# Kernel optimization log

Hardware: AMD Instinct MI355X
Metric: run time of the kernel (lower is better)

Reference implementation:

```python
import jax, jax.numpy as jnp
import numpy as np

DIM = 256
NUM_HEADS = 8
BALL_SIZE = 16
DIMENSIONALITY = 3
TOPK = 2  # hardcoded in the torch forward
NM = 8192  # n_balls(512) * ball_size(16)


def setup_inputs() -> dict:
    key = jax.random.key(0)
    ks = jax.random.split(key, 6)
    s = 0.02
    return {
        "x": jax.random.normal(ks[0], (NM, DIM), jnp.float32),
        "pos": jax.random.normal(ks[1], (NM, DIMENSIONALITY), jnp.float32),
        "W_qkv": jax.random.normal(ks[2], (3 * DIM, DIM), jnp.float32) * s,
        "b_qkv": jnp.zeros((3 * DIM,), jnp.float32),
        "W_pe": jax.random.normal(ks[3], (DIM, DIMENSIONALITY), jnp.float32) * s,
        "b_pe": jnp.zeros((DIM,), jnp.float32),
        "W_proj": jax.random.normal(ks[4], (DIM, DIM), jnp.float32) * s,
        "b_proj": jnp.zeros((DIM,), jnp.float32),
    }


def reference(x, pos, W_qkv, b_qkv, W_pe, b_pe, W_proj, b_proj):
    M, H, K = BALL_SIZE, NUM_HEADS, TOPK
    nm, dim = x.shape
    n = nm // M
    E = dim // H

    # relative positions wrt ball center (torch version is under no_grad)
    p = jax.lax.stop_gradient(pos).reshape(n, M, -1)
    rel = (p - p.mean(axis=1, keepdims=True)).reshape(nm, -1)
    x = x + rel @ W_pe.T + b_pe

    # qkv: '(n m) (H E K) -> K n H m E'  (K is innermost in the split)
    qkv = (x @ W_qkv.T + b_qkv).reshape(n, M, H, E, 3)
    qkv = jnp.transpose(qkv, (4, 0, 2, 1, 3))  # [3, n, H, m, E]
    q, k, v = qkv[0], qkv[1], qkv[2]

    qf = jnp.transpose(q, (1, 0, 2, 3)).reshape(H, nm, E)  # H (n m) E
    kh = jnp.transpose(k, (1, 0, 2, 3))  # H n m E
    vh = jnp.transpose(v, (1, 0, 2, 3))  # H n m E

    # per-ball key means, query-ball similarity, top-k ball selection
    kmean = kh.mean(axis=2)                          # H n E
    sim = jnp.einsum('hqe,hne->hqn', qf, kmean)      # H nm n
    _, idx = jax.lax.top_k(sim, K)                   # H nm K

    # gather selected balls' keys/values per (head, query-token)
    dk = jax.vmap(lambda kk, ii: kk[ii])(kh, idx).reshape(H, nm, K * M, E)
    dv = jax.vmap(lambda vv, ii: vv[ii])(vh, idx).reshape(H, nm, K * M, E)

    logits = jnp.einsum('hqe,hqke->hqk', qf, dk) / jnp.sqrt(jnp.float32(E))
    attn = jax.nn.softmax(logits, axis=-1)           # H nm (K*m)
    out = jnp.einsum('hqk,hqke->hqe', attn, dv)      # H nm E
    out = jnp.transpose(out, (1, 0, 2)).reshape(nm, dim)  # nm (H E)
    return out @ W_proj.T + b_proj
```

## Files before the change

### kernel.cpp

```cpp
#include <hip/hip_runtime.h>

#define DIM 256
#define NH 8
#define HE 32
#define BALL 16
#define NBALLS 512
#define NM 8192

typedef _Float16 f16x8 __attribute__((ext_vector_type(8)));
typedef float f32x4 __attribute__((ext_vector_type(4)));

__device__ __forceinline__ void f2h_split(float val, _Float16& hi,
                                          _Float16& lo) {
  hi = (_Float16)val;
  lo = (_Float16)(val - (float)hi);
}

__device__ __forceinline__ void gld_lds16(_Float16* lds, const _Float16* g) {
  __builtin_amdgcn_global_load_lds(
      (const __attribute__((address_space(1))) unsigned int*)g,
      (__attribute__((address_space(3))) unsigned int*)lds, 16, 0, 0);
}

__global__ __launch_bounds__(256) void k_prep(
    const float* __restrict__ x, const float* __restrict__ pos,
    const float* __restrict__ Wpe, const float* __restrict__ bpe,
    _Float16* __restrict__ xcat, const float* __restrict__ Wq,
    const float* __restrict__ Wp, _Float16* __restrict__ Bq,
    _Float16* __restrict__ Bp) {
  if (blockIdx.x >= NBALLS) {
    int n = blockIdx.x - NBALLS;
    int k = threadIdx.x;
    if (n < 768) {
      _Float16 hi, lo;
      f2h_split(Wq[n * 256 + k], hi, lo);
      Bq[n * 768 + k] = hi;
      Bq[n * 768 + 256 + k] = hi;
      Bq[n * 768 + 512 + k] = lo;
    } else {
      int r = n - 768;
      _Float16 hi, lo;
      f2h_split(Wp[r * 256 + k], hi, lo);
      Bp[r * 768 + k] = hi;
      Bp[r * 768 + 256 + k] = hi;
      Bp[r * 768 + 512 + k] = lo;
    }
    return;
  }
  __shared__ float ps[BALL * 3];
  __shared__ float mean_s[3];
  int ball = blockIdx.x;
  int tid = threadIdx.x;
  if (tid < BALL * 3) ps[tid] = pos[ball * BALL * 3 + tid];
  __syncthreads();
  if (tid < 3) {
    float s = 0.f;
    for (int m = 0; m < BALL; ++m) s += ps[m * 3 + tid];
    mean_s[tid] = s * (1.f / BALL);
  }
  __syncthreads();
  int d = tid;
  float w0 = Wpe[d * 3 + 0], w1 = Wpe[d * 3 + 1], w2 = Wpe[d * 3 + 2];
  float bp = bpe[d];
  float m0 = mean_s[0], m1 = mean_s[1], m2 = mean_s[2];
  for (int m = 0; m < BALL; ++m) {
    int t = ball * BALL + m;
    float r0 = ps[m * 3 + 0] - m0;
    float r1 = ps[m * 3 + 1] - m1;
    float r2 = ps[m * 3 + 2] - m2;
    float val = x[t * DIM + d] + r0 * w0 + r1 * w1 + r2 * w2 + bp;
    _Float16 hi, lo;
    f2h_split(val, hi, lo);
    xcat[t * 512 + d] = hi;
    xcat[t * 512 + 256 + d] = lo;
  }
}

#define TBK 64

template <typename AF, typename BF, typename Epi>
__device__ __forceinline__ void gemm_core(AF a_addr, BF b_addr,
                                          const float* __restrict__ bias,
                                          int m0, int n0, Epi epi) {
  __shared__ _Float16 As[128 * 64];
  __shared__ _Float16 Bs[64 * 64];
  int tid = threadIdx.x;
  int w = tid >> 6, lane = tid & 63;
  int wm = (w >> 1) * 64, wn = (w & 1) * 32;
  int l15 = lane & 15, quad = lane >> 4;
  int sw = l15 & 7;
  f32x4 acc[4][2] = {};
  for (int k0 = 0; k0 < 768; k0 += TBK) {
    int ak0 = (k0 < 512) ? k0 : (k0 - 512);
    if (k0) __syncthreads();
#pragma unroll
    for (int t = 0; t < 4; ++t) {
      int f = tid + 256 * t;
      int row = f >> 3, sg = (f & 7) ^ (row & 7);
      gld_lds16(&As[f * 8], a_addr(m0 + row, ak0 + sg * 8));
    }
#pragma unroll
    for (int t = 0; t < 2; ++t) {
      int f = tid + 256 * t;
      int row = f >> 3, sg = (f & 7) ^ (row & 7);
      gld_lds16(&Bs[f * 8], b_addr(n0 + row, k0 + sg * 8));
    }
    __syncthreads();
#pragma unroll
    for (int kk = 0; kk < TBK; kk += 32) {
      int ls = (kk >> 3) + quad;
      int psg = (ls ^ sw) * 8;
      f16x8 bfr0 = *(const f16x8*)&Bs[(wn + l15) * 64 + psg];
      f16x8 bfr1 = *(const f16x8*)&Bs[(wn + 16 + l15) * 64 + psg];
#pragma unroll
      for (int mt = 0; mt < 4; ++mt) {
        f16x8 afr = *(const f16x8*)&As[(wm + mt * 16 + l15) * 64 + psg];
        acc[mt][0] = __builtin_amdgcn_mfma_f32_16x16x32_f16(afr, bfr0,
                                                            acc[mt][0], 0, 0,
                                                            0);
        acc[mt][1] = __builtin_amdgcn_mfma_f32_16x16x32_f16(afr, bfr1,
                                                            acc[mt][1], 0, 0,
                                                            0);
      }
    }
  }
#pragma unroll
  for (int mt = 0; mt < 4; ++mt) {
#pragma unroll
    for (int nt = 0; nt < 2; ++nt) {
      int col = n0 + wn + nt * 16 + l15;
      float bv = bias[col];
#pragma unroll
      for (int r = 0; r < 4; ++r) {
        int row = m0 + wm + mt * 16 + quad * 4 + r;
        epi(row, col, acc[mt][nt][r] + bv);
      }
    }
  }
}

__global__ __launch_bounds__(256) void k_qkv_gemm(
    const _Float16* __restrict__ A, const _Float16* __restrict__ B,
    const float* __restrict__ bias, _Float16* __restrict__ qcat,
    float* __restrict__ kbuf, _Float16* __restrict__ kv16) {
  int m0 = blockIdx.x * 128, n0 = blockIdx.y * 64;
  gemm_core(
      [=](int r, int k) { return &A[r * 512 + k]; },
      [=](int r, int k) { return &B[r * 768 + k]; }, bias, m0, n0,
      [=](int row, int col, float val) {
        int c = col % 3;
        int rr = col / 3;
        int e = rr & 31;
        int h = rr >> 5;
        if (c == 0) {
          _Float16 hi, lo;
          f2h_split(val, hi, lo);
          qcat[(h * NM + row) * 64 + e] = hi;
          qcat[(h * NM + row) * 64 + 32 + e] = lo;
        } else if (c == 1) {
          kbuf[(h * NM + row) * HE + e] = val;
          kv16[(h * NM + row) * 64 + e] = (_Float16)val;
        } else {
          kv16[(h * NM + row) * 64 + 32 + e] = (_Float16)val;
        }
      });
}

__global__ __launch_bounds__(256) void k_proj(
    const _Float16* __restrict__ acat, const _Float16* __restrict__ B,
    const float* __restrict__ bias, float* __restrict__ out) {
  int m0 = blockIdx.x * 128, n0 = blockIdx.y * 64;
  gemm_core(
      [=](int r, int k) {
        int half = k >> 8, hh = (k >> 5) & 7, e0 = k & 31;
        return &acat[((half * NH + hh) * NM + r) * 32 + e0];
      },
      [=](int r, int k) { return &B[r * 768 + k]; }, bias, m0, n0,
      [=](int row, int col, float val) { out[row * DIM + col] = val; });
}

__global__ __launch_bounds__(256) void k_kmean(
    const float* __restrict__ kbuf, _Float16* __restrict__ kmc) {
  int tid = threadIdx.x;
  int gb = blockIdx.x * 8 + (tid >> 5);
  int e = tid & 31;
  int h = gb >> 9, ball = gb & 511;
  float s = 0.f;
#pragma unroll
  for (int m = 0; m < BALL; ++m)
    s += kbuf[(h * NM + ball * BALL + m) * HE + e];
  float mean = s * (1.f / BALL);
  _Float16 hi, lo;
  f2h_split(mean, hi, lo);
  kmc[gb * 64 + e] = hi;
  kmc[gb * 64 + 32 + e] = lo;
}

__global__ __launch_bounds__(512) void k_sim_topk(
    const _Float16* __restrict__ qcat, const _Float16* __restrict__ kmc,
    int2* __restrict__ topk2) {
  __shared__ _Float16 km_s[128 * 64];
  int tid = threadIdx.x;
  int h = blockIdx.y;
  int wv = tid >> 6, lane = tid & 63;
  int l15 = lane & 15, quad = lane >> 4;
  int sw = l15 & 7;
  int q0 = blockIdx.x * 128 + wv * 16;

  const _Float16* qr = &qcat[(h * NM + q0 + l15) * 64];
  f16x8 qhi = *(const f16x8*)&qr[quad * 8];
  f16x8 qlo = *(const f16x8*)&qr[32 + quad * 8];

  float v0[4], v1[4];
  int i0[4], i1[4];
#pragma unroll
  for (int r = 0; r < 4; ++r) {
    v0[r] = -1e30f; v1[r] = -1e30f; i0[r] = 0; i1[r] = 0;
  }

  for (int ch = 0; ch < 4; ++ch) {
    if (ch) __syncthreads();
#pragma unroll
    for (int t = 0; t < 2; ++t) {
      int f = tid + 512 * t;
      int row = f >> 3, sg = (f & 7) ^ (row & 7);
      gld_lds16(&km_s[f * 8],
                &kmc[(h * NBALLS + ch * 128 + row) * 64 + sg * 8]);
    }
    __syncthreads();

#pragma unroll
    for (int tile = 0; tile < 8; ++tile) {
      const _Float16* bb = &km_s[(tile * 16 + l15) * 64];
      f16x8 bhi = *(const f16x8*)&bb[(quad ^ sw) * 8];
      f16x8 blo = *(const f16x8*)&bb[((4 + quad) ^ sw) * 8];
      f32x4 acc = {};
      acc = __builtin_amdgcn_mfma_f32_16x16x32_f16(qhi, bhi, acc, 0, 0, 0);
      acc = __builtin_amdgcn_mfma_f32_16x16x32_f16(qlo, bhi, acc, 0, 0, 0);
      acc = __builtin_amdgcn_mfma_f32_16x16x32_f16(qhi, blo, acc, 0, 0, 0);
      int ball = ch * 128 + tile * 16 + l15;
#pragma unroll
      for (int r = 0; r < 4; ++r) {
        float s = acc[r];
        bool gt0 = s > v0[r];
        bool gt1 = s > v1[r];
        float nv1 = gt0 ? v0[r] : (gt1 ? s : v1[r]);
        int ni1 = gt0 ? i0[r] : (gt1 ? ball : i1[r]);
        v0[r] = gt0 ? s : v0[r];
        i0[r] = gt0 ? ball : i0[r];
        v1[r] = nv1;
        i1[r] = ni1;
      }
    }
  }

#pragma unroll
  for (int m = 1; m < 16; m <<= 1) {
#pragma unroll
    for (int r = 0; r < 4; ++r) {
      float w0 = __shfl_xor(v0[r], m), w1 = __shfl_xor(v1[r], m);
      int j0 = __shfl_xor(i0[r], m), j1 = __shfl_xor(i1[r], m);
      bool a = w0 > v0[r];
      float c2v = a ? v0[r] : w0;
      int c2i = a ? i0[r] : j0;
      float o2v = a ? w1 : v1[r];
      int o2i = a ? j1 : i1[r];
      v0[r] = a ? w0 : v0[r];
      i0[r] = a ? j0 : i0[r];
      bool b2 = c2v > o2v;
      v1[r] = b2 ? c2v : o2v;
      i1[r] = b2 ? c2i : o2i;
    }
  }
  if (l15 == 0) {
#pragma unroll
    for (int r = 0; r < 4; ++r) {
      int q = q0 + quad * 4 + r;
      topk2[h * NM + q] = make_int2(i0[r], i1[r]);
    }
  }
}

__global__ __launch_bounds__(256) void k_attn(
    const _Float16* __restrict__ qcat, const _Float16* __restrict__ kv16,
    const int2* __restrict__ topk2, _Float16* __restrict__ acat) {
  __shared__ _Float16 kv_s[4][32 * 72];
  __shared__ float q_s[4][HE];
  __shared__ float attw[4][32];
  int wv = threadIdx.x >> 6;
  int tid = threadIdx.x & 63;
  int idx = blockIdx.x * 4 + wv;
  int h = idx >> 13, t = idx & (NM - 1);

  int2 tk = topk2[h * NM + t];

  if (tid < HE) {
    const _Float16* qr = &qcat[(h * NM + t) * 64];
    q_s[wv][tid] = (float)qr[tid] + (float)qr[32 + tid];
  }
#pragma unroll
  for (int i = 0; i < 4; ++i) {
    int g = tid + 64 * i;
    int j = g >> 3, seg = g & 7;
    int ball = (j < 16) ? tk.x : tk.y;
    int m = j & 15;
    *(uint4*)&kv_s[wv][j * 72 + seg * 8] =
        *(const uint4*)&kv16[(h * NM + ball * BALL + m) * 64 + seg * 8];
  }
  __syncthreads();

  int j = tid & 31, half = tid >> 5;
  int e0 = half * 16;
  float partial = 0.f;
  {
    f16x8 ka = *(const f16x8*)&kv_s[wv][j * 72 + e0];
    f16x8 kb = *(const f16x8*)&kv_s[wv][j * 72 + e0 + 8];
#pragma unroll
    for (int e = 0; e < 8; ++e) {
      partial += q_s[wv][e0 + e] * (float)ka[e];
      partial += q_s[wv][e0 + 8 + e] * (float)kb[e];
    }
  }
  partial += __shfl_xor(partial, 32);
  float logit = partial * 0.17677669529663687f;
  float mx = logit;
#pragma unroll
  for (int mk = 1; mk <= 16; mk <<= 1) mx = fmaxf(mx, __shfl_xor(mx, mk));
  float pexp = __expf(logit - mx);
  float sum = pexp;
#pragma unroll
  for (int mk = 1; mk <= 16; mk <<= 1) sum += __shfl_xor(sum, mk);
  float attn = pexp / sum;
  if (tid < 32) attw[wv][j] = attn;
  __syncthreads();

  int e = tid & 31, j0 = half * 16;
  float po = 0.f;
#pragma unroll
  for (int jj = 0; jj < 16; ++jj)
    po += attw[wv][j0 + jj] * (float)kv_s[wv][(j0 + jj) * 72 + 32 + e];
  po += __shfl_xor(po, 32);
  if (tid < 32) {
    _Float16 hi, lo;
    f2h_split(po, hi, lo);
    acat[(h * NM + t) * 32 + e] = hi;
    acat[((NH + h) * NM + t) * 32 + e] = lo;
  }
}

extern "C" void kernel_launch(void* const* d_in, const int* in_sizes, int n_in,
                              void* d_out, int out_size, void* d_ws,
                              size_t ws_size, hipStream_t stream) {
  const float* x = (const float*)d_in[0];
  const float* pos = (const float*)d_in[1];
  const float* Wqkv = (const float*)d_in[2];
  const float* bqkv = (const float*)d_in[3];
  const float* Wpe = (const float*)d_in[4];
  const float* bpe = (const float*)d_in[5];
  const float* Wproj = (const float*)d_in[6];
  const float* bproj = (const float*)d_in[7];
  float* out = (float*)d_out;

  float* kbuf = (float*)d_ws;
  _Float16* kv16 = (_Float16*)(kbuf + NH * NM * HE);
  _Float16* qcat = kv16 + NH * NM * 64;
  _Float16* kmc = qcat + NH * NM * 64;
  int2* topk2 = (int2*)(kmc + NH * NBALLS * 64);
  _Float16* xcat = (_Float16*)(topk2 + NH * NM);
  _Float16* acat = xcat + NM * 512;
  _Float16* Bq = acat + 2 * NH * NM * 32;
  _Float16* Bp = Bq + 768 * 768;

  k_prep<<<NBALLS + 1024, 256, 0, stream>>>(x, pos, Wpe, bpe, xcat, Wqkv,
                                            Wproj, Bq, Bp);
  k_qkv_gemm<<<dim3(NM / 128, 768 / 64), 256, 0, stream>>>(xcat, Bq, bqkv,
                                                           qcat, kbuf, kv16);
  k_kmean<<<(NH * NBALLS) / 8, 256, 0, stream>>>(kbuf, kmc);
  k_sim_topk<<<dim3(NM / 128, NH), 512, 0, stream>>>(qcat, kmc, topk2);
  k_attn<<<NH * NM / 4, 256, 0, stream>>>(qcat, kv16, topk2, acat);
  k_proj<<<dim3(NM / 128, DIM / 64), 256, 0, stream>>>(acat, Bp, bproj, out);
}
```

Baseline: 154.3 us.

## Fuse per-ball key mean into QKV GEMM epilogue and permute weight rows

Reorders the QKV weight rows so each GEMM column block holds only q, k or v, which makes the epilogue branch uniform across a block. The k-block epilogue now reduces the 16 rows of each ball with lane shuffles and writes the ball mean directly. This removes the separate k_kmean kernel and the fp32 kbuf write and read. The risk is more epilogue work and register pressure in the GEMM.

Result: faster. 145.6 us (median of 2 runs) (-5.7%).

```diff
diff --git a/kernel.cpp b/kernel.cpp
--- a/kernel.cpp
+++ b/kernel.cpp
@@ -32,11 +32,14 @@
     int n = blockIdx.x - NBALLS;
     int k = threadIdx.x;
     if (n < 768) {
+      int c = n % 3, rr = n / 3;
+      int e = rr & 31, h = rr >> 5;
+      int np = c * 256 + h * 32 + e;
       _Float16 hi, lo;
       f2h_split(Wq[n * 256 + k], hi, lo);
-      Bq[n * 768 + k] = hi;
-      Bq[n * 768 + 256 + k] = hi;
-      Bq[n * 768 + 512 + k] = lo;
+      Bq[np * 768 + k] = hi;
+      Bq[np * 768 + 256 + k] = hi;
+      Bq[np * 768 + 512 + k] = lo;
     } else {
       int r = n - 768;
       _Float16 hi, lo;
@@ -79,9 +82,8 @@
 #define TBK 64
 
 template <typename AF, typename BF, typename Epi>
-__device__ __forceinline__ void gemm_core(AF a_addr, BF b_addr,
-                                          const float* __restrict__ bias,
-                                          int m0, int n0, Epi epi) {
+__device__ __forceinline__ void gemm_core(AF a_addr, BF b_addr, int m0,
+                                          int n0, Epi epi) {
   __shared__ _Float16 As[128 * 64];
   __shared__ _Float16 Bs[64 * 64];
   int tid = threadIdx.x;
@@ -124,44 +126,64 @@
       }
     }
   }
-#pragma unroll
-  for (int mt = 0; mt < 4; ++mt) {
-#pragma unroll
-    for (int nt = 0; nt < 2; ++nt) {
-      int col = n0 + wn + nt * 16 + l15;
-      float bv = bias[col];
-#pragma unroll
-      for (int r = 0; r < 4; ++r) {
-        int row = m0 + wm + mt * 16 + quad * 4 + r;
-        epi(row, col, acc[mt][nt][r] + bv);
-      }
-    }
-  }
+  epi(acc, wm, wn, l15, quad);
 }
 
 __global__ __launch_bounds__(256) void k_qkv_gemm(
     const _Float16* __restrict__ A, const _Float16* __restrict__ B,
     const float* __restrict__ bias, _Float16* __restrict__ qcat,
-    float* __restrict__ kbuf, _Float16* __restrict__ kv16) {
+    _Float16* __restrict__ kmc, _Float16* __restrict__ kv16) {
   int m0 = blockIdx.x * 128, n0 = blockIdx.y * 64;
+  int c = n0 >> 8;
   gemm_core(
       [=](int r, int k) { return &A[r * 512 + k]; },
-      [=](int r, int k) { return &B[r * 768 + k]; }, bias, m0, n0,
-      [=](int row, int col, float val) {
-        int c = col % 3;
-        int rr = col / 3;
-        int e = rr & 31;
-        int h = rr >> 5;
-        if (c == 0) {
-          _Float16 hi, lo;
-          f2h_split(val, hi, lo);
-          qcat[(h * NM + row) * 64 + e] = hi;
-          qcat[(h * NM + row) * 64 + 32 + e] = lo;
-        } else if (c == 1) {
-          kbuf[(h * NM + row) * HE + e] = val;
-          kv16[(h * NM + row) * 64 + e] = (_Float16)val;
-        } else {
-          kv16[(h * NM + row) * 64 + 32 + e] = (_Float16)val;
+      [=](int r, int k) { return &B[r * 768 + k]; }, m0, n0,
+      [=](f32x4 (&acc)[4][2], int wm, int wn, int l15, int quad) {
+#pragma unroll
+        for (int nt = 0; nt < 2; ++nt) {
+          int col = n0 + wn + nt * 16 + l15;
+          int cc = col & 255;
+          int e = cc & 31, h = cc >> 5;
+          float bv = bias[h * 96 + e * 3 + c];
+#pragma unroll
+          for (int mt = 0; mt < 4; ++mt) {
+            int rb = m0 + wm + mt * 16;
+            if (c == 0) {
+#pragma unroll
+              for (int r = 0; r < 4; ++r) {
+                int row = rb + quad * 4 + r;
+                _Float16 hi, lo;
+                f2h_split(acc[mt][nt][r] + bv, hi, lo);
+                qcat[(h * NM + row) * 64 + e] = hi;
+                qcat[(h * NM + row) * 64 + 32 + e] = lo;
+              }
+            } else if (c == 1) {
+              float s = 0.f;
+#pragma unroll
+              for (int r = 0; r < 4; ++r) {
+                int row = rb + quad * 4 + r;
+                float val = acc[mt][nt][r] + bv;
+                kv16[(h * NM + row) * 64 + e] = (_Float16)val;
+                s += acc[mt][nt][r];
+              }
+              s += __shfl_xor(s, 16);
+              s += __shfl_xor(s, 32);
+              if (quad == 0) {
+                int ball = rb >> 4;
+                _Float16 hi, lo;
+                f2h_split(s * (1.f / BALL) + bv, hi, lo);
+                kmc[(h * NBALLS + ball) * 64 + e] = hi;
+                kmc[(h * NBALLS + ball) * 64 + 32 + e] = lo;
+              }
+            } else {
+#pragma unroll
+              for (int r = 0; r < 4; ++r) {
+                int row = rb + quad * 4 + r;
+                kv16[(h * NM + row) * 64 + 32 + e] =
+                    (_Float16)(acc[mt][nt][r] + bv);
+              }
+            }
+          }
         }
       });
 }
@@ -175,25 +197,22 @@
         int half = k >> 8, hh = (k >> 5) & 7, e0 = k & 31;
         return &acat[((half * NH + hh) * NM + r) * 32 + e0];
       },
-      [=](int r, int k) { return &B[r * 768 + k]; }, bias, m0, n0,
-      [=](int row, int col, float val) { out[row * DIM + col] = val; });
-}
-
-__global__ __launch_bounds__(256) void k_kmean(
-    const float* __restrict__ kbuf, _Float16* __restrict__ kmc) {
-  int tid = threadIdx.x;
-  int gb = blockIdx.x * 8 + (tid >> 5);
-  int e = tid & 31;
-  int h = gb >> 9, ball = gb & 511;
-  float s = 0.f;
-#pragma unroll
-  for (int m = 0; m < BALL; ++m)
-    s += kbuf[(h * NM + ball * BALL + m) * HE + e];
-  float mean = s * (1.f / BALL);
-  _Float16 hi, lo;
-  f2h_split(mean, hi, lo);
-  kmc[gb * 64 + e] = hi;
-  kmc[gb * 64 + 32 + e] = lo;
+      [=](int r, int k) { return &B[r * 768 + k]; }, m0, n0,
+      [=](f32x4 (&acc)[4][2], int wm, int wn, int l15, int quad) {
+#pragma unroll
+        for (int nt = 0; nt < 2; ++nt) {
+          int col = n0 + wn + nt * 16 + l15;
+          float bv = bias[col];
+#pragma unroll
+          for (int mt = 0; mt < 4; ++mt) {
+#pragma unroll
+            for (int r = 0; r < 4; ++r) {
+              int row = m0 + wm + mt * 16 + quad * 4 + r;
+              out[row * DIM + col] = acc[mt][nt][r] + bv;
+            }
+          }
+        }
+      });
 }
 
 __global__ __launch_bounds__(512) void k_sim_topk(
@@ -361,8 +380,7 @@
   const float* bproj = (const float*)d_in[7];
   float* out = (float*)d_out;
 
-  float* kbuf = (float*)d_ws;
-  _Float16* kv16 = (_Float16*)(kbuf + NH * NM * HE);
+  _Float16* kv16 = (_Float16*)d_ws;
   _Float16* qcat = kv16 + NH * NM * 64;
   _Float16* kmc = qcat + NH * NM * 64;
   int2* topk2 = (int2*)(kmc + NH * NBALLS * 64);
@@ -374,8 +392,7 @@
   k_prep<<<NBALLS + 1024, 256, 0, stream>>>(x, pos, Wpe, bpe, xcat, Wqkv,
                                             Wproj, Bq, Bp);
   k_qkv_gemm<<<dim3(NM / 128, 768 / 64), 256, 0, stream>>>(xcat, Bq, bqkv,
-                                                           qcat, kbuf, kv16);
-  k_kmean<<<(NH * NBALLS) / 8, 256, 0, stream>>>(kbuf, kmc);
+                                                           qcat, kmc, kv16);
   k_sim_topk<<<dim3(NM / 128, NH), 512, 0, stream>>>(qcat, kmc, topk2);
   k_attn<<<NH * NM / 4, 256, 0, stream>>>(qcat, kv16, topk2, acat);
   k_proj<<<dim3(NM / 128, DIM / 64), 256, 0, stream>>>(acat, Bp, bproj, out);
```
